# Optimization experiments

Hardware: AMD Instinct MI355X
Metric: run time of the kernel (lower is better)

## Reference

```python
import jax, jax.numpy as jnp
import numpy as np

EMBED_DIM = 768
NUM_HEADS = 12
HEAD_DIM = EMBED_DIM // NUM_HEADS
SCALE = HEAD_DIM ** -0.5
EPS = 1e-5


def _layernorm(x, g, b):
    m = jnp.mean(x, axis=-1, keepdims=True)
    v = jnp.mean(jnp.square(x - m), axis=-1, keepdims=True)
    return (x - m) * jax.lax.rsqrt(v + EPS) * g + b


def setup_inputs() -> dict:
    key = jax.random.key(0)
    ks = jax.random.split(key, 8)
    B, N, D, Hd = 16, 1024, EMBED_DIM, HEAD_DIM
    x = jax.random.normal(ks[0], (B, N, D), dtype=jnp.float32)
    W_qkv = jax.random.normal(ks[1], (D, 3 * D), dtype=jnp.float32) * (D ** -0.5)
    b_qkv = jnp.zeros((3 * D,), dtype=jnp.float32)
    W_proj = jax.random.normal(ks[2], (D, D), dtype=jnp.float32) * (D ** -0.5)
    b_proj = jnp.zeros((D,), dtype=jnp.float32)
    return {
        "x": x,
        "ln_g": jnp.ones((D,), jnp.float32), "ln_b": jnp.zeros((D,), jnp.float32),
        "W_qkv": W_qkv, "b_qkv": b_qkv,
        "qn_g": jnp.ones((Hd,), jnp.float32), "qn_b": jnp.zeros((Hd,), jnp.float32),
        "kn_g": jnp.ones((Hd,), jnp.float32), "kn_b": jnp.zeros((Hd,), jnp.float32),
        "W_proj": W_proj, "b_proj": b_proj,
    }


def reference(x, ln_g, ln_b, W_qkv, b_qkv, qn_g, qn_b, kn_g, kn_b, W_proj, b_proj):
    B, N, D = x.shape
    H, Hd = NUM_HEADS, HEAD_DIM
    xn = _layernorm(x, ln_g, ln_b)                      # qkv_norm (pre-LN of embed_dim)
    qkv = xn @ W_qkv + b_qkv                            # [B,N,3D]
    qkv = qkv.reshape(B, N, 3, H, Hd)
    q = jnp.transpose(qkv[:, :, 0], (0, 2, 1, 3))       # [B,H,N,Hd]
    k = jnp.transpose(qkv[:, :, 1], (0, 2, 1, 3))
    v = jnp.transpose(qkv[:, :, 2], (0, 2, 1, 3))
    q = _layernorm(q, qn_g, qn_b)                       # per-head QK LayerNorm
    k = _layernorm(k, kn_g, kn_b)
    attn = jnp.einsum("bhnd,bhmd->bhnm", q, k) * SCALE
    attn = jax.nn.softmax(attn, axis=-1)
    out = jnp.einsum("bhnm,bhmd->bhnd", attn, v)        # [B,H,N,Hd]
    out = jnp.transpose(out, (0, 2, 1, 3)).reshape(B, N, D)
    return out @ W_proj + b_proj
```

## Files before the change

kernel.cpp:

```cpp
#include <hip/hip_runtime.h>

typedef _Float16 half8 __attribute__((ext_vector_type(8)));
typedef _Float16 half4 __attribute__((ext_vector_type(4)));
typedef _Float16 half2v __attribute__((ext_vector_type(2)));
typedef float f32x4 __attribute__((ext_vector_type(4)));

#define B_    16
#define N_    1024
#define D_    768
#define H_    12
#define M_    (B_ * N_)
#define QKVN_ 2304
#define EPS_  1e-5f
#define QS_   0.18033688011112042f

__device__ __forceinline__ float exp2_fast(float x) {
#if __has_builtin(__builtin_amdgcn_exp2f)
    return __builtin_amdgcn_exp2f(x);
#else
    return __builtin_exp2f(x);
#endif
}

__device__ __forceinline__ void gl16(const _Float16* g, _Float16* l) {
    __builtin_amdgcn_global_load_lds((const __attribute__((address_space(1))) void*)g,
                                     (__attribute__((address_space(3))) void*)l, 16, 0, 0);
}

__global__ __launch_bounds__(256) void convert_w(const float* __restrict__ Wqkv,
                                                 const float* __restrict__ Wproj,
                                                 _Float16* __restrict__ wqkvT,
                                                 _Float16* __restrict__ wprojT) {
    __shared__ float T[64][65];
    int t = blockIdx.x;
    const float* W; _Float16* O; int NW, k0, n0;
    if (t < 432) { W = Wqkv;  O = wqkvT;  NW = QKVN_; k0 = (t % 12) * 64; n0 = (t / 12) * 64; }
    else { t -= 432; W = Wproj; O = wprojT; NW = D_;  k0 = (t % 12) * 64; n0 = (t / 12) * 64; }
    int c = threadIdx.x & 63, r4 = threadIdx.x >> 6;
#pragma unroll
    for (int i = 0; i < 16; ++i) {
        int r = i * 4 + r4;
        T[r][c] = W[(size_t)(k0 + r) * NW + n0 + c];
    }
    __syncthreads();
#pragma unroll
    for (int i = 0; i < 16; ++i) {
        int r = i * 4 + r4;
        O[(size_t)(n0 + r) * D_ + k0 + c] = (_Float16)T[c][r];
    }
}

__global__ __launch_bounds__(256) void ln_embed(const float* __restrict__ x,
                                                const float* __restrict__ g,
                                                const float* __restrict__ bb,
                                                _Float16* __restrict__ xn) {
    int row = blockIdx.x;
    int tid = threadIdx.x;
    const float2* xr = (const float2*)(x + (size_t)row * D_);
    float2 v0 = xr[tid];
    float2 v1 = make_float2(0.f, 0.f);
    if (tid < 128) v1 = xr[256 + tid];
    float s = v0.x + v0.y + v1.x + v1.y;
    float q = v0.x * v0.x + v0.y * v0.y + v1.x * v1.x + v1.y * v1.y;
#pragma unroll
    for (int m = 32; m >= 1; m >>= 1) {
        s += __shfl_xor(s, m);
        q += __shfl_xor(q, m);
    }
    __shared__ float ss[4], qq[4];
    int wave = tid >> 6;
    if ((tid & 63) == 0) { ss[wave] = s; qq[wave] = q; }
    __syncthreads();
    float S = ss[0] + ss[1] + ss[2] + ss[3];
    float Q = qq[0] + qq[1] + qq[2] + qq[3];
    float mean = S * (1.f / 768.f);
    float var  = Q * (1.f / 768.f) - mean * mean;
    float rstd = rsqrtf(var + EPS_);
    const float2* g2 = (const float2*)g;
    const float2* b2 = (const float2*)bb;
    half2v* xo = (half2v*)(xn + (size_t)row * D_);
    {
        float2 ga = g2[tid], ba = b2[tid];
        half2v w;
        w[0] = (_Float16)((v0.x - mean) * rstd * ga.x + ba.x);
        w[1] = (_Float16)((v0.y - mean) * rstd * ga.y + ba.y);
        xo[tid] = w;
    }
    if (tid < 128) {
        float2 ga = g2[256 + tid], ba = b2[256 + tid];
        half2v w;
        w[0] = (_Float16)((v1.x - mean) * rstd * ga.x + ba.x);
        w[1] = (_Float16)((v1.y - mean) * rstd * ga.y + ba.y);
        xo[256 + tid] = w;
    }
}

__global__ __launch_bounds__(256) void gemm_qkv(const _Float16* __restrict__ A,
                                                const _Float16* __restrict__ BT,
                                                const float* __restrict__ bias,
                                                const float* __restrict__ qn_g,
                                                const float* __restrict__ qn_b,
                                                const float* __restrict__ kn_g,
                                                const float* __restrict__ kn_b,
                                                _Float16* __restrict__ qo,
                                                _Float16* __restrict__ ko,
                                                _Float16* __restrict__ vt) {
    __shared__ _Float16 As[3][128 * 32];
    __shared__ _Float16 Bs[3][128 * 32];
    const int K = D_;
    int xcd = blockIdx.x & 7, loc = blockIdx.x >> 3;
    int m0 = (xcd * 16 + loc / 18) * 128;
    int n0 = (loc % 18) * 128;
    int tid = threadIdx.x;
    int wave = tid >> 6, lane = tid & 63;
    int wm = wave >> 1, wn = wave & 1;
    int lg = lane >> 4, l15 = lane & 15;
    int xorr = (l15 >> 1) & 3;

    auto stage = [&](int buf, int tstep) {
        int k0 = tstep * 32;
#pragma unroll
        for (int i = 0; i < 2; ++i) {
            int cb = (i * 4 + wave) * 64;
            int chunk = cb + lane;
            int r = chunk >> 2, c = chunk & 3;
            int cg = c ^ ((r >> 1) & 3);
            gl16(&A[(size_t)(m0 + r) * K + k0 + cg * 8], &As[buf][cb * 8]);
            gl16(&BT[(size_t)(n0 + r) * K + k0 + cg * 8], &Bs[buf][cb * 8]);
        }
    };

    f32x4 acc[4][4] = {};
    stage(0, 0); stage(1, 1); stage(2, 2);
    for (int t = 0; t < 24; ++t) {
        int cur = t % 3;
        asm volatile("s_waitcnt vmcnt(8)" ::: "memory");
        __builtin_amdgcn_s_barrier();
        const _Float16* asb = As[cur];
        const _Float16* bsb = Bs[cur];
        half8 af[4], bf[4];
#pragma unroll
        for (int i = 0; i < 4; ++i) {
            af[i] = *(const half8*)&asb[(wm * 64 + i * 16 + l15) * 32 + (lg ^ xorr) * 8];
            bf[i] = *(const half8*)&bsb[(wn * 64 + i * 16 + l15) * 32 + (lg ^ xorr) * 8];
        }
#pragma unroll
        for (int mi = 0; mi < 4; ++mi)
#pragma unroll
            for (int ni = 0; ni < 4; ++ni)
                acc[mi][ni] = __builtin_amdgcn_mfma_f32_16x16x32_f16(af[mi], bf[ni], acc[mi][ni], 0, 0, 0);
        __builtin_amdgcn_sched_barrier(0);
        __builtin_amdgcn_s_barrier();
        stage(cur, (t + 3) % 24);
    }

    int col0 = n0 + wn * 64;
    int s = col0 / 768;
    int hcol = (col0 % 768) >> 6;
    float qkvb[4];
#pragma unroll
    for (int ni = 0; ni < 4; ++ni) qkvb[ni] = bias[col0 + ni * 16 + l15];

    if (s == 2) {
#pragma unroll
        for (int mi = 0; mi < 4; ++mi) {
            int r0 = m0 + wm * 64 + mi * 16 + lg * 4;
            int bidx = r0 >> 10, pos = r0 & 1023;
            int kvblk = pos >> 5, h = (pos >> 4) & 1, lgR = (pos >> 2) & 3;
            size_t vbase = ((size_t)(bidx * H_ + hcol) * 32 + kvblk) * 4;
#pragma unroll
            for (int ni = 0; ni < 4; ++ni) {
                half4 h4;
#pragma unroll
                for (int j = 0; j < 4; ++j) h4[j] = (_Float16)(acc[mi][ni][j] + qkvb[ni]);
                *(half4*)&vt[(vbase + ni) * 512 + lgR * 128 + l15 * 8 + h * 4] = h4;
            }
        }
    } else {
        const float* gg = (s == 0) ? qn_g : kn_g;
        const float* bb = (s == 0) ? qn_b : kn_b;
        float gv[4], bv[4];
#pragma unroll
        for (int ni = 0; ni < 4; ++ni) { gv[ni] = gg[ni * 16 + l15]; bv[ni] = bb[ni * 16 + l15]; }
#pragma unroll
        for (int mi = 0; mi < 4; ++mi) {
#pragma unroll
            for (int j = 0; j < 4; ++j) {
                float v[4];
                float sm = 0.f, sq = 0.f;
#pragma unroll
                for (int ni = 0; ni < 4; ++ni) {
                    v[ni] = acc[mi][ni][j] + qkvb[ni];
                    sm += v[ni];
                    sq += v[ni] * v[ni];
                }
#pragma unroll
                for (int msk = 1; msk < 16; msk <<= 1) {
                    sm += __shfl_xor(sm, msk);
                    sq += __shfl_xor(sq, msk);
                }
                float mean = sm * (1.f / 64.f);
                float var  = sq * (1.f / 64.f) - mean * mean;
                float rstd = rsqrtf(var + EPS_);
                int row = m0 + wm * 64 + mi * 16 + lg * 4 + j;
                int bidx = row >> 10, pos = row & 1023;
                if (s == 0) {
                    size_t rbase = ((size_t)(bidx * H_ + hcol) * 1024 + pos) * 64;
#pragma unroll
                    for (int ni = 0; ni < 4; ++ni) {
                        float o = (v[ni] - mean) * rstd * gv[ni] + bv[ni];
                        qo[rbase + ni * 16 + l15] = (_Float16)(o * QS_);
                    }
                } else {
                    int kvblk = pos >> 5, nh = (pos >> 4) & 1, l15R = pos & 15;
                    size_t base2 = ((size_t)(bidx * H_ + hcol) * 32 + kvblk) * 4 + nh * 2;
#pragma unroll
                    for (int ni = 0; ni < 4; ++ni) {
                        float o = (v[ni] - mean) * rstd * gv[ni] + bv[ni];
                        int ks = ni >> 1, lgR = ((ni & 1) << 1) | (l15 >> 3), elem = l15 & 7;
                        ko[(base2 + ks) * 512 + lgR * 128 + l15R * 8 + elem] = (_Float16)o;
                    }
                }
            }
        }
    }
}

struct KV {
    half8 kf[2][2];
    half8 vf[4];
};

__device__ __forceinline__ void ldKV(KV& s, const _Float16* kp, const _Float16* vp, int kvblk) {
    const _Float16* kb = kp + (size_t)kvblk * 2048;
#pragma unroll
    for (int nh = 0; nh < 2; ++nh)
#pragma unroll
        for (int ks = 0; ks < 2; ++ks)
            s.kf[nh][ks] = *(const half8*)(kb + (nh * 2 + ks) * 512);
    const _Float16* vb = vp + (size_t)kvblk * 2048;
#pragma unroll
    for (int di = 0; di < 4; ++di)
        s.vf[di] = *(const half8*)(vb + di * 512);
}

__device__ __forceinline__ void blockKV(const KV& s, const half8 (&qf)[4][2],
                                        f32x4 (&oacc)[4][4], f32x4 (&lacc)[4],
                                        half8 ones) {
#pragma unroll
    for (int mi = 0; mi < 4; ++mi) {
        f32x4 a0 = {}, a1 = {};
#pragma unroll
        for (int ks = 0; ks < 2; ++ks) {
            a0 = __builtin_amdgcn_mfma_f32_16x16x32_f16(s.kf[0][ks], qf[mi][ks], a0, 0, 0, 0);
            a1 = __builtin_amdgcn_mfma_f32_16x16x32_f16(s.kf[1][ks], qf[mi][ks], a1, 0, 0, 0);
        }
        half8 pf;
#pragma unroll
        for (int j = 0; j < 4; ++j) {
            pf[j]     = (_Float16)exp2_fast(a0[j]);
            pf[j + 4] = (_Float16)exp2_fast(a1[j]);
        }
        lacc[mi] = __builtin_amdgcn_mfma_f32_16x16x32_f16(ones, pf, lacc[mi], 0, 0, 0);
#pragma unroll
        for (int di = 0; di < 4; ++di)
            oacc[mi][di] = __builtin_amdgcn_mfma_f32_16x16x32_f16(s.vf[di], pf, oacc[mi][di], 0, 0, 0);
    }
}

__global__ __launch_bounds__(128, 2) void attn(const _Float16* __restrict__ qg,
                                               const _Float16* __restrict__ kg,
                                               const _Float16* __restrict__ vtg,
                                               _Float16* __restrict__ o) {
    int bphys = blockIdx.x;
    int jj = (bphys & 7) * 192 + (bphys >> 3);
    int bh = jj >> 3, qt = jj & 7;
    int b = bh / H_, h = bh % H_;
    int tid = threadIdx.x;
    int wid = tid >> 6, lane = tid & 63;
    int lg = lane >> 4, l15 = lane & 15;
    size_t base = (size_t)bh << 10;
    int qw0 = qt * 128 + wid * 64;

    const _Float16* qrow = qg + (base + qw0 + l15) * 64 + lg * 8;
    half8 qf[4][2];
#pragma unroll
    for (int mi = 0; mi < 4; ++mi)
#pragma unroll
        for (int ks = 0; ks < 2; ++ks)
            qf[mi][ks] = *(const half8*)(qrow + mi * 1024 + ks * 32);

    const _Float16* kp = kg + (size_t)bh * 65536 + lane * 8;
    const _Float16* vp = vtg + (size_t)bh * 65536 + lane * 8;

    half8 ones;
#pragma unroll
    for (int i = 0; i < 8; ++i) ones[i] = (_Float16)1.0f;

    f32x4 oacc[4][4] = {};
    f32x4 lacc[4] = {};

    KV s0, s1;
    ldKV(s0, kp, vp, 0);
    for (int t = 0; t < 16; ++t) {
        ldKV(s1, kp, vp, (2 * t + 1) & 31);
        blockKV(s0, qf, oacc, lacc, ones);
        ldKV(s0, kp, vp, (2 * t + 2) & 31);
        blockKV(s1, qf, oacc, lacc, ones);
    }

#pragma unroll
    for (int mi = 0; mi < 4; ++mi) {
        float inv = 1.f / lacc[mi][0];
        int q = qw0 + mi * 16 + l15;
        size_t rowb = ((size_t)(b * N_ + q)) * D_ + h * 64 + lg * 4;
#pragma unroll
        for (int di = 0; di < 4; ++di) {
            half4 h4;
#pragma unroll
            for (int j = 0; j < 4; ++j) h4[j] = (_Float16)(oacc[mi][di][j] * inv);
            *(half4*)&o[rowb + di * 16] = h4;
        }
    }
}

__global__ __launch_bounds__(256) void gemm_proj(const _Float16* __restrict__ A,
                                                 const _Float16* __restrict__ BT,
                                                 const float* __restrict__ bias,
                                                 float* __restrict__ out) {
    __shared__ _Float16 As[3][128 * 32];
    __shared__ _Float16 Bs[3][128 * 32];
    const int K = D_;
    int xcd = blockIdx.x & 7, loc = blockIdx.x >> 3;
    int m0 = (xcd * 16 + loc / 6) * 128;
    int n0 = (loc % 6) * 128;
    int tid = threadIdx.x;
    int wave = tid >> 6, lane = tid & 63;
    int wm = wave >> 1, wn = wave & 1;
    int lg = lane >> 4, l15 = lane & 15;
    int xorr = (l15 >> 1) & 3;

    auto stage = [&](int buf, int tstep) {
        int k0 = tstep * 32;
#pragma unroll
        for (int i = 0; i < 2; ++i) {
            int cb = (i * 4 + wave) * 64;
            int chunk = cb + lane;
            int r = chunk >> 2, c = chunk & 3;
            int cg = c ^ ((r >> 1) & 3);
            gl16(&A[(size_t)(m0 + r) * K + k0 + cg * 8], &As[buf][cb * 8]);
            gl16(&BT[(size_t)(n0 + r) * K + k0 + cg * 8], &Bs[buf][cb * 8]);
        }
    };

    f32x4 acc[4][4] = {};
    stage(0, 0); stage(1, 1); stage(2, 2);
    for (int t = 0; t < 24; ++t) {
        int cur = t % 3;
        asm volatile("s_waitcnt vmcnt(8)" ::: "memory");
        __builtin_amdgcn_s_barrier();
        const _Float16* asb = As[cur];
        const _Float16* bsb = Bs[cur];
        half8 af[4], bf[4];
#pragma unroll
        for (int i = 0; i < 4; ++i) {
            af[i] = *(const half8*)&asb[(wm * 64 + i * 16 + l15) * 32 + (lg ^ xorr) * 8];
            bf[i] = *(const half8*)&bsb[(wn * 64 + i * 16 + l15) * 32 + (lg ^ xorr) * 8];
        }
#pragma unroll
        for (int mi = 0; mi < 4; ++mi)
#pragma unroll
            for (int ni = 0; ni < 4; ++ni)
                acc[mi][ni] = __builtin_amdgcn_mfma_f32_16x16x32_f16(af[mi], bf[ni], acc[mi][ni], 0, 0, 0);
        __builtin_amdgcn_sched_barrier(0);
        __builtin_amdgcn_s_barrier();
        stage(cur, (t + 3) % 24);
    }
#pragma unroll
    for (int mi = 0; mi < 4; ++mi)
#pragma unroll
        for (int ni = 0; ni < 4; ++ni) {
            int col = n0 + wn * 64 + ni * 16 + l15;
            float bv = bias[col];
#pragma unroll
            for (int j = 0; j < 4; ++j) {
                int row = m0 + wm * 64 + mi * 16 + lg * 4 + j;
                out[(size_t)row * D_ + col] = acc[mi][ni][j] + bv;
            }
        }
}

extern "C" void kernel_launch(void* const* d_in, const int* in_sizes, int n_in,
                              void* d_out, int out_size, void* d_ws, size_t ws_size,
                              hipStream_t stream) {
    const float* x      = (const float*)d_in[0];
    const float* ln_g   = (const float*)d_in[1];
    const float* ln_b   = (const float*)d_in[2];
    const float* W_qkv  = (const float*)d_in[3];
    const float* b_qkv  = (const float*)d_in[4];
    const float* qn_g   = (const float*)d_in[5];
    const float* qn_b   = (const float*)d_in[6];
    const float* kn_g   = (const float*)d_in[7];
    const float* kn_b   = (const float*)d_in[8];
    const float* W_proj = (const float*)d_in[9];
    const float* b_proj = (const float*)d_in[10];
    float* out = (float*)d_out;
    char* ws = (char*)d_ws;

    constexpr size_t XN_SZ    = (size_t)M_ * D_ * 2;
    constexpr size_t WQKVT_SZ = (size_t)QKVN_ * D_ * 2;
    constexpr size_t WPROJT_SZ= (size_t)D_ * D_ * 2;
    constexpr size_t HEAD_SZ  = (size_t)B_ * H_ * N_ * 64 * 2;

    _Float16* xn     = (_Float16*)(ws);
    _Float16* wqkvT  = (_Float16*)(ws + XN_SZ);
    _Float16* wprojT = (_Float16*)(ws + XN_SZ + WQKVT_SZ);
    _Float16* qb     = (_Float16*)(ws + XN_SZ + WQKVT_SZ + WPROJT_SZ);
    _Float16* kb     = (_Float16*)((char*)qb + HEAD_SZ);
    _Float16* vtb    = (_Float16*)((char*)kb + HEAD_SZ);
    _Float16* ao     = xn;

    convert_w<<<576, 256, 0, stream>>>(W_qkv, W_proj, wqkvT, wprojT);
    ln_embed<<<M_, 256, 0, stream>>>(x, ln_g, ln_b, xn);
    gemm_qkv<<<M_ / 128 * (QKVN_ / 128), 256, 0, stream>>>(xn, wqkvT, b_qkv,
                                                           qn_g, qn_b, kn_g, kn_b,
                                                           qb, kb, vtb);
    attn<<<B_ * H_ * (N_ / 128), 128, 0, stream>>>(qb, kb, vtb, ao);
    gemm_proj<<<M_ / 128 * (D_ / 128), 256, 0, stream>>>(ao, wprojT, b_proj, out);
}
```

Measured before the change: 234.2 us.

## Pre-pack GEMM operands in MFMA fragment order and load directly to registers

The weights, the layernormed activations and the attention output are now written in a packed layout that matches the 16x16x32 MFMA fragment order. This lets both GEMMs read operands straight from global memory into registers with register double-buffering, with no LDS staging and no barriers. The aim is to remove LDS traffic and synchronisation. In exchange, each wave loads its own copy of the data with no intra-block sharing through LDS, relying on L2/L1 for reuse. The weight conversion also becomes scattered 2-byte writes.

```diff
diff --git a/kernel.cpp b/kernel.cpp
--- a/kernel.cpp
+++ b/kernel.cpp
@@ -22,38 +22,26 @@
 #endif
 }
 
-__device__ __forceinline__ void gl16(const _Float16* g, _Float16* l) {
-    __builtin_amdgcn_global_load_lds((const __attribute__((address_space(1))) void*)g,
-                                     (__attribute__((address_space(3))) void*)l, 16, 0, 0);
+__device__ __forceinline__ size_t pk(int t16, int kc, int lg, int p, int e) {
+    return ((size_t)(t16 * 24 + kc) * 4 + lg) * 128 + p * 8 + e;
 }
 
 __global__ __launch_bounds__(256) void convert_w(const float* __restrict__ Wqkv,
                                                  const float* __restrict__ Wproj,
-                                                 _Float16* __restrict__ wqkvT,
-                                                 _Float16* __restrict__ wprojT) {
-    __shared__ float T[64][65];
-    int t = blockIdx.x;
-    const float* W; _Float16* O; int NW, k0, n0;
-    if (t < 432) { W = Wqkv;  O = wqkvT;  NW = QKVN_; k0 = (t % 12) * 64; n0 = (t / 12) * 64; }
-    else { t -= 432; W = Wproj; O = wprojT; NW = D_;  k0 = (t % 12) * 64; n0 = (t / 12) * 64; }
-    int c = threadIdx.x & 63, r4 = threadIdx.x >> 6;
-#pragma unroll
-    for (int i = 0; i < 16; ++i) {
-        int r = i * 4 + r4;
-        T[r][c] = W[(size_t)(k0 + r) * NW + n0 + c];
-    }
-    __syncthreads();
-#pragma unroll
-    for (int i = 0; i < 16; ++i) {
-        int r = i * 4 + r4;
-        O[(size_t)(n0 + r) * D_ + k0 + c] = (_Float16)T[c][r];
-    }
+                                                 _Float16* __restrict__ wqkv_p,
+                                                 _Float16* __restrict__ wproj_p) {
+    int idx = blockIdx.x * 256 + threadIdx.x;
+    const int n1 = D_ * QKVN_;
+    int k, n; float v; _Float16* dst;
+    if (idx < n1) { k = idx / QKVN_; n = idx % QKVN_; v = Wqkv[idx]; dst = wqkv_p; }
+    else { int r = idx - n1; k = r / D_; n = r % D_; v = Wproj[r]; dst = wproj_p; }
+    dst[pk(n >> 4, k >> 5, (k >> 3) & 3, n & 15, k & 7)] = (_Float16)v;
 }
 
 __global__ __launch_bounds__(256) void ln_embed(const float* __restrict__ x,
                                                 const float* __restrict__ g,
                                                 const float* __restrict__ bb,
-                                                _Float16* __restrict__ xn) {
+                                                _Float16* __restrict__ xp) {
     int row = blockIdx.x;
     int tid = threadIdx.x;
     const float2* xr = (const float2*)(x + (size_t)row * D_);
@@ -78,82 +66,79 @@
     float rstd = rsqrtf(var + EPS_);
     const float2* g2 = (const float2*)g;
     const float2* b2 = (const float2*)bb;
-    half2v* xo = (half2v*)(xn + (size_t)row * D_);
+    int mt = row >> 4, p = row & 15;
     {
+        int d0 = 2 * tid;
         float2 ga = g2[tid], ba = b2[tid];
         half2v w;
         w[0] = (_Float16)((v0.x - mean) * rstd * ga.x + ba.x);
         w[1] = (_Float16)((v0.y - mean) * rstd * ga.y + ba.y);
-        xo[tid] = w;
+        *(half2v*)&xp[pk(mt, d0 >> 5, (d0 >> 3) & 3, p, d0 & 7)] = w;
     }
     if (tid < 128) {
+        int d0 = 512 + 2 * tid;
         float2 ga = g2[256 + tid], ba = b2[256 + tid];
         half2v w;
         w[0] = (_Float16)((v1.x - mean) * rstd * ga.x + ba.x);
         w[1] = (_Float16)((v1.y - mean) * rstd * ga.y + ba.y);
-        xo[256 + tid] = w;
-    }
-}
-
-__global__ __launch_bounds__(256) void gemm_qkv(const _Float16* __restrict__ A,
-                                                const _Float16* __restrict__ BT,
-                                                const float* __restrict__ bias,
-                                                const float* __restrict__ qn_g,
-                                                const float* __restrict__ qn_b,
-                                                const float* __restrict__ kn_g,
-                                                const float* __restrict__ kn_b,
-                                                _Float16* __restrict__ qo,
-                                                _Float16* __restrict__ ko,
-                                                _Float16* __restrict__ vt) {
-    __shared__ _Float16 As[3][128 * 32];
-    __shared__ _Float16 Bs[3][128 * 32];
-    const int K = D_;
+        *(half2v*)&xp[pk(mt, d0 >> 5, (d0 >> 3) & 3, p, d0 & 7)] = w;
+    }
+}
+
+__global__ __launch_bounds__(256, 3) void gemm_qkv(const _Float16* __restrict__ Ap,
+                                                   const _Float16* __restrict__ Bp,
+                                                   const float* __restrict__ bias,
+                                                   const float* __restrict__ qn_g,
+                                                   const float* __restrict__ qn_b,
+                                                   const float* __restrict__ kn_g,
+                                                   const float* __restrict__ kn_b,
+                                                   _Float16* __restrict__ qo,
+                                                   _Float16* __restrict__ ko,
+                                                   _Float16* __restrict__ vt) {
     int xcd = blockIdx.x & 7, loc = blockIdx.x >> 3;
-    int m0 = (xcd * 16 + loc / 18) * 128;
-    int n0 = (loc % 18) * 128;
+    int mt0 = (xcd * 16 + loc / 18) * 8;
+    int nt0 = (loc % 18) * 8;
     int tid = threadIdx.x;
     int wave = tid >> 6, lane = tid & 63;
     int wm = wave >> 1, wn = wave & 1;
     int lg = lane >> 4, l15 = lane & 15;
-    int xorr = (l15 >> 1) & 3;
-
-    auto stage = [&](int buf, int tstep) {
-        int k0 = tstep * 32;
-#pragma unroll
-        for (int i = 0; i < 2; ++i) {
-            int cb = (i * 4 + wave) * 64;
-            int chunk = cb + lane;
-            int r = chunk >> 2, c = chunk & 3;
-            int cg = c ^ ((r >> 1) & 3);
-            gl16(&A[(size_t)(m0 + r) * K + k0 + cg * 8], &As[buf][cb * 8]);
-            gl16(&BT[(size_t)(n0 + r) * K + k0 + cg * 8], &Bs[buf][cb * 8]);
+
+    const _Float16* pa[4];
+    const _Float16* pb[4];
+#pragma unroll
+    for (int i = 0; i < 4; ++i) {
+        pa[i] = Ap + (size_t)(mt0 + wm * 4 + i) * 12288 + lane * 8;
+        pb[i] = Bp + (size_t)(nt0 + wn * 4 + i) * 12288 + lane * 8;
+    }
+    f32x4 acc[4][4] = {};
+    half8 a0[4], b0[4], a1[4], b1[4];
+    auto ld = [&](half8 (&a)[4], half8 (&b)[4], int t) {
+        int off = t * 512;
+#pragma unroll
+        for (int i = 0; i < 4; ++i) {
+            a[i] = *(const half8*)(pa[i] + off);
+            b[i] = *(const half8*)(pb[i] + off);
         }
     };
-
-    f32x4 acc[4][4] = {};
-    stage(0, 0); stage(1, 1); stage(2, 2);
-    for (int t = 0; t < 24; ++t) {
-        int cur = t % 3;
-        asm volatile("s_waitcnt vmcnt(8)" ::: "memory");
-        __builtin_amdgcn_s_barrier();
-        const _Float16* asb = As[cur];
-        const _Float16* bsb = Bs[cur];
-        half8 af[4], bf[4];
-#pragma unroll
-        for (int i = 0; i < 4; ++i) {
-            af[i] = *(const half8*)&asb[(wm * 64 + i * 16 + l15) * 32 + (lg ^ xorr) * 8];
-            bf[i] = *(const half8*)&bsb[(wn * 64 + i * 16 + l15) * 32 + (lg ^ xorr) * 8];
-        }
+    auto mm = [&](half8 (&a)[4], half8 (&b)[4]) {
 #pragma unroll
         for (int mi = 0; mi < 4; ++mi)
 #pragma unroll
             for (int ni = 0; ni < 4; ++ni)
-                acc[mi][ni] = __builtin_amdgcn_mfma_f32_16x16x32_f16(af[mi], bf[ni], acc[mi][ni], 0, 0, 0);
-        __builtin_amdgcn_sched_barrier(0);
-        __builtin_amdgcn_s_barrier();
-        stage(cur, (t + 3) % 24);
-    }
-
+                acc[mi][ni] = __builtin_amdgcn_mfma_f32_16x16x32_f16(a[mi], b[ni], acc[mi][ni], 0, 0, 0);
+    };
+    ld(a0, b0, 0);
+    for (int tt = 0; tt < 11; ++tt) {
+        ld(a1, b1, 2 * tt + 1);
+        mm(a0, b0);
+        ld(a0, b0, 2 * tt + 2);
+        mm(a1, b1);
+    }
+    ld(a1, b1, 23);
+    mm(a0, b0);
+    mm(a1, b1);
+
+    int m0 = mt0 * 16, n0 = nt0 * 16;
     int col0 = n0 + wn * 64;
     int s = col0 / 768;
     int hcol = (col0 % 768) >> 6;
@@ -271,7 +256,7 @@
 __global__ __launch_bounds__(128, 2) void attn(const _Float16* __restrict__ qg,
                                                const _Float16* __restrict__ kg,
                                                const _Float16* __restrict__ vtg,
-                                               _Float16* __restrict__ o) {
+                                               _Float16* __restrict__ op) {
     int bphys = blockIdx.x;
     int jj = (bphys & 7) * 192 + (bphys >> 3);
     int bh = jj >> 3, qt = jj & 7;
@@ -312,70 +297,65 @@
 #pragma unroll
     for (int mi = 0; mi < 4; ++mi) {
         float inv = 1.f / lacc[mi][0];
-        int q = qw0 + mi * 16 + l15;
-        size_t rowb = ((size_t)(b * N_ + q)) * D_ + h * 64 + lg * 4;
+        int mt = b * 64 + (qw0 >> 4) + mi;
 #pragma unroll
         for (int di = 0; di < 4; ++di) {
             half4 h4;
 #pragma unroll
             for (int j = 0; j < 4; ++j) h4[j] = (_Float16)(oacc[mi][di][j] * inv);
-            *(half4*)&o[rowb + di * 16] = h4;
-        }
-    }
-}
-
-__global__ __launch_bounds__(256) void gemm_proj(const _Float16* __restrict__ A,
-                                                 const _Float16* __restrict__ BT,
-                                                 const float* __restrict__ bias,
-                                                 float* __restrict__ out) {
-    __shared__ _Float16 As[3][128 * 32];
-    __shared__ _Float16 Bs[3][128 * 32];
-    const int K = D_;
+            *(half4*)&op[pk(mt, 2 * h + (di >> 1), (di & 1) * 2 + (lg >> 1), l15, (lg & 1) * 4)] = h4;
+        }
+    }
+}
+
+__global__ __launch_bounds__(256, 3) void gemm_proj(const _Float16* __restrict__ Ap,
+                                                    const _Float16* __restrict__ Bp,
+                                                    const float* __restrict__ bias,
+                                                    float* __restrict__ out) {
     int xcd = blockIdx.x & 7, loc = blockIdx.x >> 3;
-    int m0 = (xcd * 16 + loc / 6) * 128;
-    int n0 = (loc % 6) * 128;
+    int mt0 = (xcd * 16 + loc / 6) * 8;
+    int nt0 = (loc % 6) * 8;
     int tid = threadIdx.x;
     int wave = tid >> 6, lane = tid & 63;
     int wm = wave >> 1, wn = wave & 1;
     int lg = lane >> 4, l15 = lane & 15;
-    int xorr = (l15 >> 1) & 3;
-
-    auto stage = [&](int buf, int tstep) {
-        int k0 = tstep * 32;
-#pragma unroll
-        for (int i = 0; i < 2; ++i) {
-            int cb = (i * 4 + wave) * 64;
-            int chunk = cb + lane;
-            int r = chunk >> 2, c = chunk & 3;
-            int cg = c ^ ((r >> 1) & 3);
-            gl16(&A[(size_t)(m0 + r) * K + k0 + cg * 8], &As[buf][cb * 8]);
-            gl16(&BT[(size_t)(n0 + r) * K + k0 + cg * 8], &Bs[buf][cb * 8]);
+
+    const _Float16* pa[4];
+    const _Float16* pb[4];
+#pragma unroll
+    for (int i = 0; i < 4; ++i) {
+        pa[i] = Ap + (size_t)(mt0 + wm * 4 + i) * 12288 + lane * 8;
+        pb[i] = Bp + (size_t)(nt0 + wn * 4 + i) * 12288 + lane * 8;
+    }
+    f32x4 acc[4][4] = {};
+    half8 a0[4], b0[4], a1[4], b1[4];
+    auto ld = [&](half8 (&a)[4], half8 (&b)[4], int t) {
+        int off = t * 512;
+#pragma unroll
+        for (int i = 0; i < 4; ++i) {
+            a[i] = *(const half8*)(pa[i] + off);
+            b[i] = *(const half8*)(pb[i] + off);
         }
     };
-
-    f32x4 acc[4][4] = {};
-    stage(0, 0); stage(1, 1); stage(2, 2);
-    for (int t = 0; t < 24; ++t) {
-        int cur = t % 3;
-        asm volatile("s_waitcnt vmcnt(8)" ::: "memory");
-        __builtin_amdgcn_s_barrier();
-        const _Float16* asb = As[cur];
-        const _Float16* bsb = Bs[cur];
-        half8 af[4], bf[4];
-#pragma unroll
-        for (int i = 0; i < 4; ++i) {
-            af[i] = *(const half8*)&asb[(wm * 64 + i * 16 + l15) * 32 + (lg ^ xorr) * 8];
-            bf[i] = *(const half8*)&bsb[(wn * 64 + i * 16 + l15) * 32 + (lg ^ xorr) * 8];
-        }
+    auto mm = [&](half8 (&a)[4], half8 (&b)[4]) {
 #pragma unroll
         for (int mi = 0; mi < 4; ++mi)
 #pragma unroll
             for (int ni = 0; ni < 4; ++ni)
-                acc[mi][ni] = __builtin_amdgcn_mfma_f32_16x16x32_f16(af[mi], bf[ni], acc[mi][ni], 0, 0, 0);
-        __builtin_amdgcn_sched_barrier(0);
-        __builtin_amdgcn_s_barrier();
-        stage(cur, (t + 3) % 24);
-    }
+                acc[mi][ni] = __builtin_amdgcn_mfma_f32_16x16x32_f16(a[mi], b[ni], acc[mi][ni], 0, 0, 0);
+    };
+    ld(a0, b0, 0);
+    for (int tt = 0; tt < 11; ++tt) {
+        ld(a1, b1, 2 * tt + 1);
+        mm(a0, b0);
+        ld(a0, b0, 2 * tt + 2);
+        mm(a1, b1);
+    }
+    ld(a1, b1, 23);
+    mm(a0, b0);
+    mm(a1, b1);
+
+    int m0 = mt0 * 16, n0 = nt0 * 16;
 #pragma unroll
     for (int mi = 0; mi < 4; ++mi)
 #pragma unroll
@@ -412,19 +392,19 @@
     constexpr size_t WPROJT_SZ= (size_t)D_ * D_ * 2;
     constexpr size_t HEAD_SZ  = (size_t)B_ * H_ * N_ * 64 * 2;
 
-    _Float16* xn     = (_Float16*)(ws);
-    _Float16* wqkvT  = (_Float16*)(ws + XN_SZ);
-    _Float16* wprojT = (_Float16*)(ws + XN_SZ + WQKVT_SZ);
+    _Float16* xn_p   = (_Float16*)(ws);
+    _Float16* wqkv_p = (_Float16*)(ws + XN_SZ);
+    _Float16* wproj_p= (_Float16*)(ws + XN_SZ + WQKVT_SZ);
     _Float16* qb     = (_Float16*)(ws + XN_SZ + WQKVT_SZ + WPROJT_SZ);
     _Float16* kb     = (_Float16*)((char*)qb + HEAD_SZ);
     _Float16* vtb    = (_Float16*)((char*)kb + HEAD_SZ);
-    _Float16* ao     = xn;
-
-    convert_w<<<576, 256, 0, stream>>>(W_qkv, W_proj, wqkvT, wprojT);
-    ln_embed<<<M_, 256, 0, stream>>>(x, ln_g, ln_b, xn);
-    gemm_qkv<<<M_ / 128 * (QKVN_ / 128), 256, 0, stream>>>(xn, wqkvT, b_qkv,
+    _Float16* ao_p   = xn_p;
+
+    convert_w<<<9216, 256, 0, stream>>>(W_qkv, W_proj, wqkv_p, wproj_p);
+    ln_embed<<<M_, 256, 0, stream>>>(x, ln_g, ln_b, xn_p);
+    gemm_qkv<<<M_ / 128 * (QKVN_ / 128), 256, 0, stream>>>(xn_p, wqkv_p, b_qkv,
                                                            qn_g, qn_b, kn_g, kn_b,
                                                            qb, kb, vtb);
-    attn<<<B_ * H_ * (N_ / 128), 128, 0, stream>>>(qb, kb, vtb, ao);
-    gemm_proj<<<M_ / 128 * (D_ / 128), 256, 0, stream>>>(ao, wprojT, b_proj, out);
-}
+    attn<<<B_ * H_ * (N_ / 128), 128, 0, stream>>>(qb, kb, vtb, ao_p);
+    gemm_proj<<<M_ / 128 * (D_ / 128), 256, 0, stream>>>(ao_p, wproj_p, b_proj, out);
+}
```

Result: faster. 203.1 us (-13.3%).
